# Optimization experiments

Measured on AMD Instinct MI355X. Metric: run time of the kernel, lower is better.

Reference implementation:

```python
import jax, jax.numpy as jnp
import numpy as np

N_NODES = 100000


def setup_inputs() -> dict:
    key = jax.random.key(0)
    k1, k2, k3 = jax.random.split(key, 3)
    x = jax.random.normal(k1, (N_NODES, 256), dtype=jnp.float32)
    edge_index = jax.random.randint(k2, (2, 1600000), 0, N_NODES, dtype=jnp.int64)
    W = jax.random.normal(k3, (256, 128), dtype=jnp.float32) * (1.0 / np.sqrt(256.0))
    b = jnp.zeros((128,), dtype=jnp.float32)
    alpha = jnp.full((128,), 0.25, dtype=jnp.float32)  # PReLU default init
    return {"x": x, "edge_index": edge_index, "W": W, "b": b, "alpha": alpha}


def reference(x, edge_index, W, b, alpha):
    N = x.shape[0]
    # --- GCNConv: add self-loops ---
    loops = jnp.arange(N, dtype=edge_index.dtype)
    row = jnp.concatenate([edge_index[0], loops])  # source nodes
    col = jnp.concatenate([edge_index[1], loops])  # destination nodes
    # symmetric normalization: deg computed at destinations (self-loops => deg >= 1)
    deg = jax.ops.segment_sum(jnp.ones(col.shape, x.dtype), col, num_segments=N)
    dinv = jax.lax.rsqrt(deg)
    norm = dinv[row] * dinv[col]  # [E+N]
    # linear transform then normalized scatter-add aggregation
    h = x @ W  # [N, H]
    msg = h[row] * norm[:, None]  # [E+N, H]
    out = jax.ops.segment_sum(msg, col, num_segments=N) + b  # bias after aggregation
    # --- PReLU (per-channel) ---
    return jnp.where(out >= 0, out, alpha * out)
```

## Files before the change

kernel.cpp:

```cpp
#include <hip/hip_runtime.h>

constexpr int KDIM  = 256;
constexpr int HDIM  = 128;
constexpr int BK    = 128;
constexpr int CHUNK = 8192;
constexpr int NBMAX = 800;

typedef __bf16 bf16x8 __attribute__((ext_vector_type(8)));
typedef float  f32x4  __attribute__((ext_vector_type(4)));

__device__ __forceinline__ ushort f2bf(float f) {
    unsigned u = __float_as_uint(f);
    unsigned r = (u + 0x7fffu + ((u >> 16) & 1u)) >> 16;
    return (ushort)r;
}

__device__ __forceinline__ void accum8(float* a, uint4 u) {
    a[0] += __uint_as_float(u.x << 16); a[1] += __uint_as_float(u.x & 0xffff0000u);
    a[2] += __uint_as_float(u.y << 16); a[3] += __uint_as_float(u.y & 0xffff0000u);
    a[4] += __uint_as_float(u.z << 16); a[5] += __uint_as_float(u.z & 0xffff0000u);
    a[6] += __uint_as_float(u.w << 16); a[7] += __uint_as_float(u.w & 0xffff0000u);
}

__global__ __launch_bounds__(1024) void prep_sort_kernel(
    const float* __restrict__ W, ushort* __restrict__ Wt, ushort* __restrict__ hsb,
    const int* __restrict__ row, const int* __restrict__ col,
    uint* __restrict__ ebuf, int* __restrict__ histG, int* __restrict__ localOff,
    int n, int e, int nbv, int gblk) {
    __shared__ uint dst[CHUNK];
    __shared__ int hist[NBMAX], excl[NBMAX], cur[NBMAX];
    __shared__ int ws2[16];
    int b = blockIdx.x, t = threadIdx.x;
    if (b < 4) {
        int g = b * 1024 + t;
        int lane = g & 63, cn = g >> 6;
        int c = cn >> 3, nf = cn & 7;
        int ncol = nf * 16 + (lane & 15);
        int k0 = c * 32 + (lane >> 4) * 8;
        ushort* dp = Wt + (size_t)g * 8;
        #pragma unroll
        for (int j = 0; j < 8; ++j) dp[j] = f2bf(W[(k0 + j) * HDIM + ncol]);
        return;
    }
    if (b == 4) {
        if (t < HDIM) hsb[(size_t)n * HDIM + t] = 0;
        return;
    }
    int g = b - 5;
    int lane = t & 63, w = t >> 6;
    for (int i = t; i < nbv; i += 1024) hist[i] = 0;
    __syncthreads();
    int lo = g * CHUNK, hi = min(lo + CHUNK, e);
    int colr[8];
    #pragma unroll
    for (int k = 0; k < 2; ++k) {
        int i0 = lo + (k * 1024 + t) * 4;
        if (i0 + 3 < hi) {
            int4 c4 = *(const int4*)(col + i0);
            colr[k * 4 + 0] = c4.x; colr[k * 4 + 1] = c4.y;
            colr[k * 4 + 2] = c4.z; colr[k * 4 + 3] = c4.w;
            atomicAdd(&hist[c4.x >> 7], 1); atomicAdd(&hist[c4.y >> 7], 1);
            atomicAdd(&hist[c4.z >> 7], 1); atomicAdd(&hist[c4.w >> 7], 1);
        } else {
            #pragma unroll
            for (int j = 0; j < 4; ++j) {
                int i = i0 + j;
                int c = (i < hi) ? col[i] : -1;
                colr[k * 4 + j] = c;
                if (c >= 0) atomicAdd(&hist[c >> 7], 1);
            }
        }
    }
    __syncthreads();
    {
        int b0 = t * 2;
        int h0 = (b0 < nbv) ? hist[b0] : 0;
        int h1 = (b0 + 1 < nbv) ? hist[b0 + 1] : 0;
        int s = h0 + h1, incl = s;
        #pragma unroll
        for (int d = 1; d < 64; d <<= 1) { int u = __shfl_up(incl, d, 64); if (lane >= d) incl += u; }
        if (lane == 63) ws2[w] = incl;
        __syncthreads();
        int add = 0;
        #pragma unroll
        for (int i = 0; i < 16; ++i) if (i < w) add += ws2[i];
        int run = add + incl - s;
        if (b0 < nbv)     { excl[b0] = run;          cur[b0] = run; }
        if (b0 + 1 < nbv) { excl[b0 + 1] = run + h0; cur[b0 + 1] = run + h0; }
    }
    __syncthreads();
    #pragma unroll
    for (int k = 0; k < 2; ++k) {
        int i0 = lo + (k * 1024 + t) * 4;
        if (i0 + 3 < hi) {
            int4 r4 = *(const int4*)(row + i0);
            int rr[4] = {r4.x, r4.y, r4.z, r4.w};
            #pragma unroll
            for (int j = 0; j < 4; ++j) {
                int c = colr[k * 4 + j];
                int p = atomicAdd(&cur[c >> 7], 1);
                dst[p] = ((uint)rr[j] << 7) | (uint)(c & 127);
            }
        } else {
            #pragma unroll
            for (int j = 0; j < 4; ++j) {
                int i = i0 + j, c = colr[k * 4 + j];
                if (c >= 0) {
                    int p = atomicAdd(&cur[c >> 7], 1);
                    dst[p] = ((uint)row[i] << 7) | (uint)(c & 127);
                }
            }
        }
    }
    __syncthreads();
    int cnt = hi - lo;
    #pragma unroll
    for (int k = 0; k < 2; ++k) {
        int i0 = (k * 1024 + t) * 4;
        if (i0 + 3 < cnt) *(uint4*)(ebuf + lo + i0) = *(uint4*)&dst[i0];
        else for (int j = 0; j < 4; ++j) if (i0 + j < cnt) ebuf[lo + i0 + j] = dst[i0 + j];
    }
    for (int i = t; i < nbv; i += 1024) {
        histG[i * gblk + g]    = hist[i];
        localOff[i * gblk + g] = excl[i];
    }
}

__global__ __launch_bounds__(256) void scanA_kernel(const int* __restrict__ in,
                                                    int* __restrict__ partial, int n) {
    int t = threadIdx.x, base = blockIdx.x * 1024;
    int s = 0;
    #pragma unroll
    for (int j = 0; j < 4; ++j) {
        int i = base + j * 256 + t;
        if (i < n) s += in[i];
    }
    __shared__ int ws[4];
    #pragma unroll
    for (int d = 1; d < 64; d <<= 1) s += __shfl_xor(s, d, 64);
    int lane = t & 63, w = t >> 6;
    if (lane == 0) ws[w] = s;
    __syncthreads();
    if (t == 0) partial[blockIdx.x] = ws[0] + ws[1] + ws[2] + ws[3];
}

__global__ void scanB_kernel(int* __restrict__ partial, int nb) {
    int t = threadIdx.x;
    int v = (t < nb) ? partial[t] : 0;
    int orig = v;
    int lane = t & 63, w = t >> 6;
    #pragma unroll
    for (int d = 1; d < 64; d <<= 1) { int u = __shfl_up(v, d, 64); if (lane >= d) v += u; }
    __shared__ int ws[4];
    if (lane == 63) ws[w] = v;
    __syncthreads();
    int add = 0;
    #pragma unroll
    for (int i = 0; i < 4; ++i) if (i < w) add += ws[i];
    if (t < nb) partial[t] = v + add - orig;
}

__global__ __launch_bounds__(256) void scanC_kernel(const int* __restrict__ in,
                                                    const int* __restrict__ partial,
                                                    int* __restrict__ out, int n) {
    int t = threadIdx.x, base = blockIdx.x * 1024;
    int vals[4], tsum = 0;
    #pragma unroll
    for (int j = 0; j < 4; ++j) {
        int i = base + t * 4 + j;
        vals[j] = (i < n) ? in[i] : 0;
        tsum += vals[j];
    }
    int lane = t & 63, w = t >> 6;
    int incl = tsum;
    #pragma unroll
    for (int d = 1; d < 64; d <<= 1) { int u = __shfl_up(incl, d, 64); if (lane >= d) incl += u; }
    __shared__ int ws[4];
    if (lane == 63) ws[w] = incl;
    __syncthreads();
    int add = partial[blockIdx.x];
    #pragma unroll
    for (int i = 0; i < 4; ++i) if (i < w) add += ws[i];
    int run = add + incl - tsum;
    #pragma unroll
    for (int j = 0; j < 4; ++j) {
        int i = base + t * 4 + j;
        if (i < n) out[i] = run;
        run += vals[j];
    }
}

__global__ __launch_bounds__(256) void fine_kernel(const uint* __restrict__ ebuf,
                                                   const int* __restrict__ histG,
                                                   const int* __restrict__ localOff,
                                                   const int* __restrict__ histS,
                                                   uint* __restrict__ csr,
                                                   int* __restrict__ deg,
                                                   int* __restrict__ offs,
                                                   float* __restrict__ dinv,
                                                   int e, int nbv, int gblk, int n) {
    __shared__ uint elist[4096];
    __shared__ uint csrl[4096];
    __shared__ int hist[BK], excl[BK], cur[BK];
    int b = blockIdx.x, t = threadIdx.x;
    int grp = t >> 4, li = t & 15;
    int seg0 = histS[b * gblk];
    int seg1 = (b + 1 < nbv) ? histS[(b + 1) * gblk] : e;
    int cnt = min(seg1 - seg0, 4096);

    if (t < BK) { hist[t] = 0; cur[t] = 0; }
    for (int g0 = 0; g0 < gblk; g0 += 16) {
        int g = g0 + grp;
        if (g < gblk) {
            int c   = histG[b * gblk + g];
            int src = g * CHUNK + localOff[b * gblk + g];
            int dst = histS[b * gblk + g] - seg0;
            for (int i = li; i < c; i += 16) elist[dst + i] = ebuf[src + i];
        }
    }
    __syncthreads();
    for (int i = t; i < cnt; i += 256) atomicAdd(&hist[elist[i] & 127], 1);
    __syncthreads();
    if (t < 64) {
        int v0 = hist[2 * t], v1 = hist[2 * t + 1];
        int s = v0 + v1, incl = s;
        #pragma unroll
        for (int d = 1; d < 64; d <<= 1) { int u = __shfl_up(incl, d, 64); if (t >= d) incl += u; }
        int base = incl - s;
        excl[2 * t] = base; excl[2 * t + 1] = base + v0;
    }
    __syncthreads();
    for (int i = t; i < cnt; i += 256) {
        uint v = elist[i];
        int d = v & 127;
        int r = atomicAdd(&cur[d], 1);
        csrl[excl[d] + r] = v >> 7;
    }
    __syncthreads();
    for (int i = t; i < cnt; i += 256) csr[seg0 + i] = csrl[i];
    if (t < BK) {
        int node = b * BK + t;
        if (node < n) {
            int dg = hist[t];
            deg[node]  = dg;
            offs[node] = seg0 + excl[t];
            dinv[node] = rsqrtf((float)(dg + 1));
        }
    }
}


constexpr int MT = 64;
constexpr int XS_STRIDE = 264;

__global__ __launch_bounds__(256) void gemm_kernel(const float* __restrict__ x,
                                                   const ushort* __restrict__ Wt,
                                                   const float* __restrict__ dinv,
                                                   ushort* __restrict__ hsb, int n) {
    __shared__ ushort xs[MT * XS_STRIDE];
    __shared__ float sdinv[MT];
    int t = threadIdx.x, lane = t & 63, w = t >> 6;
    int row0 = blockIdx.x * MT;

    bf16x8 bfrag[8][2];
    #pragma unroll
    for (int c = 0; c < 8; ++c)
        #pragma unroll
        for (int f = 0; f < 2; ++f)
            bfrag[c][f] = *(const bf16x8*)(Wt + (size_t)(((c * 8) + (w * 2 + f)) * 64 + lane) * 8);

    #pragma unroll
    for (int i = 0; i < 16; ++i) {
        int rl = w * 16 + i;
        int gr = row0 + rl; if (gr >= n) gr = n - 1;
        float4 v = *(const float4*)(x + (size_t)gr * KDIM + lane * 4);
        ushort4 o;
        o.x = f2bf(v.x); o.y = f2bf(v.y); o.z = f2bf(v.z); o.w = f2bf(v.w);
        *(ushort4*)(xs + rl * XS_STRIDE + lane * 4) = o;
    }
    if (t < MT) { int g = row0 + t; sdinv[t] = dinv[(g < n) ? g : (n - 1)]; }
    __syncthreads();

    #pragma unroll
    for (int s = 0; s < MT / 16; ++s) {
        f32x4 acc0 = {0.f, 0.f, 0.f, 0.f}, acc1 = {0.f, 0.f, 0.f, 0.f};
        #pragma unroll
        for (int c = 0; c < 8; ++c) {
            const ushort* ap = xs + (s * 16 + (lane & 15)) * XS_STRIDE + c * 32 + (lane >> 4) * 8;
            bf16x8 afrag = *(const bf16x8*)ap;
            acc0 = __builtin_amdgcn_mfma_f32_16x16x32_bf16(afrag, bfrag[c][0], acc0, 0, 0, 0);
            acc1 = __builtin_amdgcn_mfma_f32_16x16x32_bf16(afrag, bfrag[c][1], acc1, 0, 0, 0);
        }
        #pragma unroll
        for (int reg = 0; reg < 4; ++reg) {
            int rl = s * 16 + (lane >> 4) * 4 + reg;
            int gr = row0 + rl;
            if (gr < n) {
                float d = sdinv[rl];
                int col0 = w * 32 + (lane & 15);
                hsb[(size_t)gr * HDIM + col0]      = f2bf(acc0[reg] * d);
                hsb[(size_t)gr * HDIM + col0 + 16] = f2bf(acc1[reg] * d);
            }
        }
    }
}

__global__ __launch_bounds__(256) void aggregate_kernel(
    const ushort* __restrict__ hsb, const int* __restrict__ offs,
    const int* __restrict__ deg, const uint* __restrict__ csr,
    const float* __restrict__ dinv, const float* __restrict__ b,
    const float* __restrict__ alpha, float* __restrict__ out, int n) {
    int wv = threadIdx.x >> 6, lane = threadIdx.x & 63;
    int grp = lane >> 4, li = lane & 15;
    int node = blockIdx.x * 16 + wv * 4 + grp;
    bool valid = node < n;
    int nd   = valid ? node : n;
    int base = valid ? offs[node] : 0;
    int cnt  = valid ? deg[node] : 0;
    const uint4* hs4 = (const uint4*)hsb;

    float a[8];
    #pragma unroll
    for (int i = 0; i < 8; ++i) a[i] = 0.f;

    uint4 su = hs4[(size_t)nd * 16 + li];
    accum8(a, su);

    for (int it = 0; it < cnt; it += 16) {
        int src_l = (it + li < cnt) ? (int)__builtin_nontemporal_load(csr + base + it + li) : n;

        int sA[8];
        #pragma unroll
        for (int k = 0; k < 8; ++k) sA[k] = __shfl(src_l, grp * 16 + k, 64);
        uint4 uA[8];
        #pragma unroll
        for (int k = 0; k < 8; ++k) uA[k] = hs4[(size_t)sA[k] * 16 + li];
        #pragma unroll
        for (int k = 0; k < 8; ++k) accum8(a, uA[k]);

        if (it + 8 < cnt) {
            int sB[8];
            #pragma unroll
            for (int k = 0; k < 8; ++k) sB[k] = __shfl(src_l, grp * 16 + 8 + k, 64);
            uint4 uB[8];
            #pragma unroll
            for (int k = 0; k < 8; ++k) uB[k] = hs4[(size_t)sB[k] * 16 + li];
            #pragma unroll
            for (int k = 0; k < 8; ++k) accum8(a, uB[k]);
        }
    }

    if (valid) {
        float dc = dinv[node];
        int c0 = li * 8;
        float o[8];
        #pragma unroll
        for (int i = 0; i < 8; ++i) {
            float v = fmaf(dc, a[i], b[c0 + i]);
            o[i] = v >= 0.f ? v : alpha[c0 + i] * v;
        }
        float* op = out + (size_t)node * HDIM + c0;
        f32x4 v0 = {o[0], o[1], o[2], o[3]};
        f32x4 v1 = {o[4], o[5], o[6], o[7]};
        __builtin_nontemporal_store(v0, (f32x4*)op);
        __builtin_nontemporal_store(v1, (f32x4*)(op + 4));
    }
}


extern "C" void kernel_launch(void* const* d_in, const int* in_sizes, int n_in,
                              void* d_out, int out_size, void* d_ws, size_t ws_size,
                              hipStream_t stream) {
    const float* x     = (const float*)d_in[0];
    const int*   ei    = (const int*)d_in[1];
    const float* W     = (const float*)d_in[2];
    const float* b     = (const float*)d_in[3];
    const float* alpha = (const float*)d_in[4];
    float* out = (float*)d_out;

    int E = in_sizes[1] / 2;
    int N = in_sizes[0] / KDIM;
    int NB = (N + BK - 1) / BK;
    int GBLK = (E + CHUNK - 1) / CHUNK;
    int SCAN_N = NB * GBLK;

    ushort* hsb   = (ushort*)d_ws;
    ushort* Wt    = hsb + (size_t)(N + 1) * HDIM;
    float* dinv   = (float*)(Wt + 32768);
    int* deg      = (int*)(dinv + N);
    int* offs     = deg + N;
    int* histG    = offs + N;
    int* localOff = histG + SCAN_N;
    int* histS    = localOff + SCAN_N;
    int* partial  = histS + SCAN_N;
    uint* ebuf    = (uint*)(partial + 512);
    uint* csr     = ebuf + (size_t)GBLK * CHUNK;

    const int* rowp = ei;
    const int* colp = ei + E;

    int nbScan = (SCAN_N + 1023) / 1024;

    hipLaunchKernelGGL(prep_sort_kernel, dim3(5 + GBLK), dim3(1024), 0, stream,
                       W, Wt, hsb, rowp, colp, ebuf, histG, localOff, N, E, NB, GBLK);
    hipLaunchKernelGGL(scanA_kernel, dim3(nbScan), dim3(256), 0, stream, histG, partial, SCAN_N);
    hipLaunchKernelGGL(scanB_kernel, dim3(1), dim3(256), 0, stream, partial, nbScan);
    hipLaunchKernelGGL(scanC_kernel, dim3(nbScan), dim3(256), 0, stream, histG, partial, histS, SCAN_N);
    hipLaunchKernelGGL(fine_kernel, dim3(NB), dim3(256), 0, stream,
                       ebuf, histG, localOff, histS, csr, deg, offs, dinv, E, NB, GBLK, N);
    hipLaunchKernelGGL(gemm_kernel, dim3((N + MT - 1) / MT), dim3(256), 0, stream, x, Wt, dinv, hsb, N);
    hipLaunchKernelGGL(aggregate_kernel, dim3((N + 15) / 16), dim3(256), 0, stream,
                       hsb, offs, deg, csr, dinv, b, alpha, out, N);
}
```

Measured before the change: 296.5 us.

## Merge three-pass global scan into one bucket scan with in-block segment prefix

Replaces the three-kernel scan over the full bucket×chunk histogram with one single-block kernel. That kernel computes only per-bucket totals and their exclusive offsets. Each fine_kernel block then rebuilds its per-chunk offsets with a small shared-memory prefix scan over histG. The sort chunk size is doubled so there are fewer chunks (gblk must stay ≤128 for the in-block scan). This cuts two launches and the global scan traffic, but leaves half as many prep blocks, each doing more work, and adds barriers in fine_kernel.

```diff
diff --git a/kernel.cpp b/kernel.cpp
--- a/kernel.cpp
+++ b/kernel.cpp
@@ -3,7 +3,7 @@
 constexpr int KDIM  = 256;
 constexpr int HDIM  = 128;
 constexpr int BK    = 128;
-constexpr int CHUNK = 8192;
+constexpr int CHUNK = 16384;
 constexpr int NBMAX = 800;
 
 typedef __bf16 bf16x8 __attribute__((ext_vector_type(8)));
@@ -51,9 +51,9 @@
     for (int i = t; i < nbv; i += 1024) hist[i] = 0;
     __syncthreads();
     int lo = g * CHUNK, hi = min(lo + CHUNK, e);
-    int colr[8];
-    #pragma unroll
-    for (int k = 0; k < 2; ++k) {
+    int colr[16];
+    #pragma unroll
+    for (int k = 0; k < 4; ++k) {
         int i0 = lo + (k * 1024 + t) * 4;
         if (i0 + 3 < hi) {
             int4 c4 = *(const int4*)(col + i0);
@@ -90,7 +90,7 @@
     }
     __syncthreads();
     #pragma unroll
-    for (int k = 0; k < 2; ++k) {
+    for (int k = 0; k < 4; ++k) {
         int i0 = lo + (k * 1024 + t) * 4;
         if (i0 + 3 < hi) {
             int4 r4 = *(const int4*)(row + i0);
@@ -115,7 +115,7 @@
     __syncthreads();
     int cnt = hi - lo;
     #pragma unroll
-    for (int k = 0; k < 2; ++k) {
+    for (int k = 0; k < 4; ++k) {
         int i0 = (k * 1024 + t) * 4;
         if (i0 + 3 < cnt) *(uint4*)(ebuf + lo + i0) = *(uint4*)&dst[i0];
         else for (int j = 0; j < 4; ++j) if (i0 + j < cnt) ebuf[lo + i0 + j] = dst[i0 + j];
@@ -126,74 +126,37 @@
     }
 }
 
-__global__ __launch_bounds__(256) void scanA_kernel(const int* __restrict__ in,
-                                                    int* __restrict__ partial, int n) {
-    int t = threadIdx.x, base = blockIdx.x * 1024;
-    int s = 0;
-    #pragma unroll
-    for (int j = 0; j < 4; ++j) {
-        int i = base + j * 256 + t;
-        if (i < n) s += in[i];
-    }
-    __shared__ int ws[4];
-    #pragma unroll
-    for (int d = 1; d < 64; d <<= 1) s += __shfl_xor(s, d, 64);
-    int lane = t & 63, w = t >> 6;
-    if (lane == 0) ws[w] = s;
-    __syncthreads();
-    if (t == 0) partial[blockIdx.x] = ws[0] + ws[1] + ws[2] + ws[3];
-}
-
-__global__ void scanB_kernel(int* __restrict__ partial, int nb) {
-    int t = threadIdx.x;
-    int v = (t < nb) ? partial[t] : 0;
+__global__ __launch_bounds__(1024) void bscan_kernel(const int* __restrict__ histG,
+                                                     int* __restrict__ bucketOff,
+                                                     int nbv, int gblk, int e) {
+    __shared__ int btot[NBMAX];
+    __shared__ int ws[16];
+    int t = threadIdx.x, lane = t & 63, w = t >> 6;
+    for (int b = w; b < nbv; b += 16) {
+        int s = 0;
+        for (int g = lane; g < gblk; g += 64) s += histG[b * gblk + g];
+        #pragma unroll
+        for (int d = 1; d < 64; d <<= 1) s += __shfl_xor(s, d, 64);
+        if (lane == 0) btot[b] = s;
+    }
+    __syncthreads();
+    int v = (t < nbv) ? btot[t] : 0;
     int orig = v;
-    int lane = t & 63, w = t >> 6;
     #pragma unroll
     for (int d = 1; d < 64; d <<= 1) { int u = __shfl_up(v, d, 64); if (lane >= d) v += u; }
-    __shared__ int ws[4];
     if (lane == 63) ws[w] = v;
     __syncthreads();
     int add = 0;
     #pragma unroll
-    for (int i = 0; i < 4; ++i) if (i < w) add += ws[i];
-    if (t < nb) partial[t] = v + add - orig;
-}
-
-__global__ __launch_bounds__(256) void scanC_kernel(const int* __restrict__ in,
-                                                    const int* __restrict__ partial,
-                                                    int* __restrict__ out, int n) {
-    int t = threadIdx.x, base = blockIdx.x * 1024;
-    int vals[4], tsum = 0;
-    #pragma unroll
-    for (int j = 0; j < 4; ++j) {
-        int i = base + t * 4 + j;
-        vals[j] = (i < n) ? in[i] : 0;
-        tsum += vals[j];
-    }
-    int lane = t & 63, w = t >> 6;
-    int incl = tsum;
-    #pragma unroll
-    for (int d = 1; d < 64; d <<= 1) { int u = __shfl_up(incl, d, 64); if (lane >= d) incl += u; }
-    __shared__ int ws[4];
-    if (lane == 63) ws[w] = incl;
-    __syncthreads();
-    int add = partial[blockIdx.x];
-    #pragma unroll
-    for (int i = 0; i < 4; ++i) if (i < w) add += ws[i];
-    int run = add + incl - tsum;
-    #pragma unroll
-    for (int j = 0; j < 4; ++j) {
-        int i = base + t * 4 + j;
-        if (i < n) out[i] = run;
-        run += vals[j];
-    }
+    for (int i = 0; i < 16; ++i) if (i < w) add += ws[i];
+    if (t < nbv) bucketOff[t] = v + add - orig;
+    if (t == 0)  bucketOff[nbv] = e;
 }
 
 __global__ __launch_bounds__(256) void fine_kernel(const uint* __restrict__ ebuf,
                                                    const int* __restrict__ histG,
                                                    const int* __restrict__ localOff,
-                                                   const int* __restrict__ histS,
+                                                   const int* __restrict__ bucketOff,
                                                    uint* __restrict__ csr,
                                                    int* __restrict__ deg,
                                                    int* __restrict__ offs,
@@ -202,21 +165,26 @@
     __shared__ uint elist[4096];
     __shared__ uint csrl[4096];
     __shared__ int hist[BK], excl[BK], cur[BK];
+    __shared__ int segOff[128];
     int b = blockIdx.x, t = threadIdx.x;
+    int seg0 = bucketOff[b];
+    int cnt = min(bucketOff[b + 1] - seg0, 4096);
+
+    if (t < 128) segOff[t] = (t < gblk) ? histG[b * gblk + t] : 0;
+    if (t < BK) { hist[t] = 0; cur[t] = 0; }
+    __syncthreads();
+    for (int d = 1; d < 128; d <<= 1) {
+        int v = (t < 128 && t >= d) ? segOff[t - d] : 0;
+        __syncthreads();
+        if (t < 128) segOff[t] += v;
+        __syncthreads();
+    }
     int grp = t >> 4, li = t & 15;
-    int seg0 = histS[b * gblk];
-    int seg1 = (b + 1 < nbv) ? histS[(b + 1) * gblk] : e;
-    int cnt = min(seg1 - seg0, 4096);
-
-    if (t < BK) { hist[t] = 0; cur[t] = 0; }
-    for (int g0 = 0; g0 < gblk; g0 += 16) {
-        int g = g0 + grp;
-        if (g < gblk) {
-            int c   = histG[b * gblk + g];
-            int src = g * CHUNK + localOff[b * gblk + g];
-            int dst = histS[b * gblk + g] - seg0;
-            for (int i = li; i < c; i += 16) elist[dst + i] = ebuf[src + i];
-        }
+    for (int g = grp; g < gblk; g += 16) {
+        int pre = (g == 0) ? 0 : segOff[g - 1];
+        int c   = segOff[g] - pre;
+        int src = g * CHUNK + localOff[b * gblk + g];
+        for (int i = li; i < c; i += 16) elist[pre + i] = ebuf[src + i];
     }
     __syncthreads();
     for (int i = t; i < cnt; i += 256) atomicAdd(&hist[elist[i] & 127], 1);
@@ -382,33 +350,29 @@
     int N = in_sizes[0] / KDIM;
     int NB = (N + BK - 1) / BK;
     int GBLK = (E + CHUNK - 1) / CHUNK;
-    int SCAN_N = NB * GBLK;
-
-    ushort* hsb   = (ushort*)d_ws;
-    ushort* Wt    = hsb + (size_t)(N + 1) * HDIM;
-    float* dinv   = (float*)(Wt + 32768);
-    int* deg      = (int*)(dinv + N);
-    int* offs     = deg + N;
-    int* histG    = offs + N;
-    int* localOff = histG + SCAN_N;
-    int* histS    = localOff + SCAN_N;
-    int* partial  = histS + SCAN_N;
-    uint* ebuf    = (uint*)(partial + 512);
-    uint* csr     = ebuf + (size_t)GBLK * CHUNK;
+
+    ushort* hsb    = (ushort*)d_ws;
+    ushort* Wt     = hsb + (size_t)(N + 1) * HDIM;
+    float* dinv    = (float*)(Wt + 32768);
+    int* deg       = (int*)(dinv + N);
+    int* offs      = deg + N;
+    int* histG     = offs + N;
+    int* localOff  = histG + (size_t)NB * GBLK;
+    int* bucketOff = localOff + (size_t)NB * GBLK;
+    uint* ebuf     = (uint*)(bucketOff + NB + 1);
+    uint* csr      = ebuf + (size_t)GBLK * CHUNK;
 
     const int* rowp = ei;
     const int* colp = ei + E;
 
-    int nbScan = (SCAN_N + 1023) / 1024;
-
     hipLaunchKernelGGL(prep_sort_kernel, dim3(5 + GBLK), dim3(1024), 0, stream,
                        W, Wt, hsb, rowp, colp, ebuf, histG, localOff, N, E, NB, GBLK);
-    hipLaunchKernelGGL(scanA_kernel, dim3(nbScan), dim3(256), 0, stream, histG, partial, SCAN_N);
-    hipLaunchKernelGGL(scanB_kernel, dim3(1), dim3(256), 0, stream, partial, nbScan);
-    hipLaunchKernelGGL(scanC_kernel, dim3(nbScan), dim3(256), 0, stream, histG, partial, histS, SCAN_N);
+    hipLaunchKernelGGL(bscan_kernel, dim3(1), dim3(1024), 0, stream,
+                       histG, bucketOff, NB, GBLK, E);
     hipLaunchKernelGGL(fine_kernel, dim3(NB), dim3(256), 0, stream,
-                       ebuf, histG, localOff, histS, csr, deg, offs, dinv, E, NB, GBLK, N);
-    hipLaunchKernelGGL(gemm_kernel, dim3((N + MT - 1) / MT), dim3(256), 0, stream, x, Wt, dinv, hsb, N);
+                       ebuf, histG, localOff, bucketOff, csr, deg, offs, dinv, E, NB, GBLK, N);
+    hipLaunchKernelGGL(gemm_kernel, dim3((N + MT - 1) / MT), dim3(256), 0, stream,
+                       x, Wt, dinv, hsb, N);
     hipLaunchKernelGGL(aggregate_kernel, dim3((N + 15) / 16), dim3(256), 0, stream,
                        hsb, offs, deg, csr, dinv, b, alpha, out, N);
 }
```

Result: slower. 322.7 us (+8.8%).
